# Kernel tuning notes

Measured on AMD Instinct MI355X. Metric: run time of the kernel, lower is better.

Reference implementation:

```python
import jax, jax.numpy as jnp
import numpy as np
import math

B, H, S, D = 8, 16, 1024, 64

def setup_inputs() -> dict:
    key = jax.random.key(0)
    kq, kk, kv = jax.random.split(key, 3)
    Q = jax.random.normal(kq, (B, H, S, D), dtype=jnp.float32)
    K = jax.random.normal(kk, (B, H, S, D), dtype=jnp.float32)
    V = jax.random.normal(kv, (B, H, S, D), dtype=jnp.float32)
    return {"Q": Q, "K": K, "V": V}

def reference(Q, K, V):
    d_k = K.shape[-1]
    # [B,H,S,S] attention scores
    score = jnp.einsum('bhqd,bhkd->bhqk', Q, K) / math.sqrt(d_k)
    attn = jax.nn.softmax(score, axis=-1)
    return jnp.einsum('bhqk,bhkd->bhqd', attn, V)
```

## Files before the change

### kernel.cpp

```cpp
#include <hip/hip_runtime.h>
#include <hip/hip_bf16.h>
#include <math.h>


#define S_ 1024
#define D_ 64
#define BQ 256
#define KVT 64
#define NTILE (S_ / KVT)
#define TILE_SHORTS (KVT * D_)

typedef __attribute__((ext_vector_type(8))) short bf16x8;
typedef __attribute__((ext_vector_type(4))) float f32x4;

#if __has_builtin(__builtin_amdgcn_exp2f)
#define EXP2F(x) __builtin_amdgcn_exp2f(x)
#else
#define EXP2F(x) exp2f(x)
#endif

__device__ __forceinline__ short f2bf(float f) {
    union { __hip_bfloat16 h; short s; } u;
    u.h = __float2bfloat16(f);
    return u.s;
}

__device__ __forceinline__ void gl2lds16(const short* g, short* l) {
    __builtin_amdgcn_global_load_lds(
        (const __attribute__((address_space(1))) unsigned int*)g,
        (__attribute__((address_space(3))) unsigned int*)l, 16, 0, 0);
}

__device__ __forceinline__ unsigned int pkbf(float a, float b) {
    unsigned int ua = __float_as_uint(a) + 0x8000u;
    unsigned int ub = __float_as_uint(b) + 0x8000u;
    return __builtin_amdgcn_perm(ub, ua, 0x07060302u);
}

__launch_bounds__(256)
__global__ void prepass_kernel(const float* __restrict__ K, const float* __restrict__ V,
                               short* __restrict__ Kb, short* __restrict__ Vb) {
    __shared__ __align__(16) short VtL[D_][72];
    const int tile = blockIdx.x, bh = blockIdx.y;
    const int tid = threadIdx.x;
    const int kv0 = tile * KVT;
    const size_t base = (size_t)bh * (S_ * D_);
    const float* Kp = K + base;
    const float* Vp = V + base;
    short* Kt = Kb + ((size_t)bh * NTILE + tile) * TILE_SHORTS;
    short* Vt = Vb + ((size_t)bh * NTILE + tile) * TILE_SHORTS;

    {
        const int c4 = tid & 15, g = tid >> 4;
        #pragma unroll
        for (int i = 0; i < 2; ++i) {
            const int kp = g + 16 * i;
            #pragma unroll
            for (int j = 0; j < 4; ++j) {
                const int d = c4 + 16 * j;
                float v0 = Vp[(size_t)(kv0 + 2 * kp) * D_ + d];
                float v1 = Vp[(size_t)(kv0 + 2 * kp + 1) * D_ + d];
                short2 vs; vs.x = f2bf(v0); vs.y = f2bf(v1);
                *(short2*)&VtL[d][2 * kp] = vs;
            }
        }
    }
    #pragma unroll
    for (int i = 0; i < 2; ++i) {
        const int s = tid + i * 256;
        const int mb = s >> 7, c = (s >> 6) & 1, lane = s & 63;
        const int quad = lane >> 4, l16 = lane & 15;
        const float* src = Kp + (size_t)(kv0 + mb * 16 + l16) * D_ + c * 32 + quad * 8;
        float4 a = *(const float4*)src;
        float4 b = *(const float4*)(src + 4);
        bf16x8 f;
        f[0]=f2bf(a.x); f[1]=f2bf(a.y); f[2]=f2bf(a.z); f[3]=f2bf(a.w);
        f[4]=f2bf(b.x); f[5]=f2bf(b.y); f[6]=f2bf(b.z); f[7]=f2bf(b.w);
        *(bf16x8*)&Kt[s * 8] = f;
    }
    __syncthreads();
    #pragma unroll
    for (int i = 0; i < 2; ++i) {
        const int s = tid + i * 256;
        const int t = s >> 7, c = (s >> 6) & 1, lane = s & 63;
        const int quad = lane >> 4, l16 = lane & 15;
        bf16x8 f = *(const bf16x8*)&VtL[t * 16 + l16][c * 32 + quad * 8];
        *(bf16x8*)&Vt[s * 8] = f;
    }
}

__launch_bounds__(256, 2)
__global__ void sdpa_kernel(const float* __restrict__ Q,
                            const short* __restrict__ Kb,
                            const short* __restrict__ Vb,
                            float* __restrict__ O) {
    __shared__ __align__(16) short Kbuf[2][TILE_SHORTS];
    __shared__ __align__(16) short Vbuf[2][TILE_SHORTS];
    __shared__ __align__(16) short Pfrag[4][1024];

    const int b   = blockIdx.x;
    const int bh  = (b & 7) | ((b >> 5) << 3);
    const int q0  = ((b >> 3) & 3) * BQ;
    const int tid = threadIdx.x;
    const int w = tid >> 6, lane = tid & 63;
    const int quad = lane >> 4, l16 = lane & 15;

    const size_t base = (size_t)bh * (S_ * D_);
    const float* Qp = Q + base;
    float*       Op = O + base;
    const short* Kg = Kb + (size_t)bh * NTILE * TILE_SHORTS;
    const short* Vg = Vb + (size_t)bh * NTILE * TILE_SHORTS;

    const float qs = 0.18033688011112042f;
    bf16x8 qfrag[4][2];
    #pragma unroll
    for (int nb = 0; nb < 4; ++nb) {
        const int qrow = q0 + w * 64 + nb * 16 + l16;
        #pragma unroll
        for (int c = 0; c < 2; ++c) {
            const float* src = Qp + (size_t)qrow * D_ + c * 32 + quad * 8;
            float4 a = *(const float4*)(src);
            float4 bb = *(const float4*)(src + 4);
            bf16x8 f;
            f[0]=f2bf(a.x*qs);  f[1]=f2bf(a.y*qs);  f[2]=f2bf(a.z*qs);  f[3]=f2bf(a.w*qs);
            f[4]=f2bf(bb.x*qs); f[5]=f2bf(bb.y*qs); f[6]=f2bf(bb.z*qs); f[7]=f2bf(bb.w*qs);
            qfrag[nb][c] = f;
        }
    }

    bf16x8 ones;
    #pragma unroll
    for (int i = 0; i < 8; ++i) ones[i] = (short)0x3F80;

    f32x4 l_acc[4];
    f32x4 o_acc[4][4];
    #pragma unroll
    for (int nb = 0; nb < 4; ++nb) {
        l_acc[nb] = (f32x4)0.f;
        #pragma unroll
        for (int t4 = 0; t4 < 4; ++t4)
            o_acc[nb][t4] = (f32x4)0.f;
    }

    auto stage = [&](int buf, int t) {
        const short* kt = Kg + (size_t)t * TILE_SHORTS;
        const short* vt = Vg + (size_t)t * TILE_SHORTS;
        #pragma unroll
        for (int i = 0; i < 2; ++i) {
            const int blk = i * 4 + w;
            gl2lds16(kt + (blk * 64 + lane) * 8, &Kbuf[buf][blk * 512]);
            gl2lds16(vt + (blk * 64 + lane) * 8, &Vbuf[buf][blk * 512]);
        }
    };

    stage(0, 0);
    __syncthreads();
    int cur = 0;

    #pragma unroll 1
    for (int t = 0; t < NTILE; ++t) {
        if (t + 1 < NTILE) stage(cur ^ 1, t + 1);

        bf16x8 kf[4][2], vf[4][2];
        #pragma unroll
        for (int mb = 0; mb < 4; ++mb) {
            kf[mb][0] = *(const bf16x8*)&Kbuf[cur][((mb * 2 + 0) * 64 + lane) * 8];
            kf[mb][1] = *(const bf16x8*)&Kbuf[cur][((mb * 2 + 1) * 64 + lane) * 8];
            vf[mb][0] = *(const bf16x8*)&Vbuf[cur][((mb * 2 + 0) * 64 + lane) * 8];
            vf[mb][1] = *(const bf16x8*)&Vbuf[cur][((mb * 2 + 1) * 64 + lane) * 8];
        }

        #pragma unroll
        for (int nb = 0; nb < 4; ++nb) {
            f32x4 st[4];
            #pragma unroll
            for (int mb = 0; mb < 4; ++mb) {
                f32x4 acc = (f32x4)0.f;
                acc = __builtin_amdgcn_mfma_f32_16x16x32_bf16(kf[mb][0], qfrag[nb][0], acc, 0, 0, 0);
                acc = __builtin_amdgcn_mfma_f32_16x16x32_bf16(kf[mb][1], qfrag[nb][1], acc, 0, 0, 0);
                st[mb] = acc;
            }

            #pragma unroll
            for (int mb = 0; mb < 4; ++mb) {
                float p0 = EXP2F(st[mb][0]);
                float p1 = EXP2F(st[mb][1]);
                float p2 = EXP2F(st[mb][2]);
                float p3 = EXP2F(st[mb][3]);
                uint2 pk;
                pk.x = pkbf(p0, p1);
                pk.y = pkbf(p2, p3);
                const int c  = mb >> 1;
                const int qp = (mb & 1) * 2 + (quad >> 1);
                const int j0 = (quad & 1) * 4;
                *(uint2*)&Pfrag[w][(c * 64 + qp * 16 + l16) * 8 + j0] = pk;
            }
            bf16x8 pf0 = *(const bf16x8*)&Pfrag[w][(0 * 64 + lane) * 8];
            bf16x8 pf1 = *(const bf16x8*)&Pfrag[w][(1 * 64 + lane) * 8];

            l_acc[nb] = __builtin_amdgcn_mfma_f32_16x16x32_bf16(pf0, ones, l_acc[nb], 0, 0, 0);
            l_acc[nb] = __builtin_amdgcn_mfma_f32_16x16x32_bf16(pf1, ones, l_acc[nb], 0, 0, 0);

            #pragma unroll
            for (int t4 = 0; t4 < 4; ++t4) {
                f32x4 acc = o_acc[nb][t4];
                acc = __builtin_amdgcn_mfma_f32_16x16x32_bf16(pf0, vf[t4][0], acc, 0, 0, 0);
                acc = __builtin_amdgcn_mfma_f32_16x16x32_bf16(pf1, vf[t4][1], acc, 0, 0, 0);
                o_acc[nb][t4] = acc;
            }
        }

        __syncthreads();
        cur ^= 1;
    }

    #pragma unroll
    for (int nb = 0; nb < 4; ++nb) {
        #pragma unroll
        for (int r = 0; r < 4; ++r) {
            const float inv = 1.0f / l_acc[nb][r];
            const int row = q0 + w * 64 + nb * 16 + quad * 4 + r;
            #pragma unroll
            for (int t4 = 0; t4 < 4; ++t4)
                Op[(size_t)row * D_ + t4 * 16 + l16] = o_acc[nb][t4][r] * inv;
        }
    }
}

extern "C" void kernel_launch(void* const* d_in, const int* in_sizes, int n_in,
                              void* d_out, int out_size, void* d_ws, size_t ws_size,
                              hipStream_t stream) {
    const float* Q = (const float*)d_in[0];
    const float* K = (const float*)d_in[1];
    const float* V = (const float*)d_in[2];
    float* O = (float*)d_out;

    const size_t tensor_shorts = (size_t)128 * NTILE * TILE_SHORTS;
    short* Kb = (short*)d_ws;
    short* Vb = Kb + tensor_shorts;

    dim3 pgrid(NTILE, 8 * 16);
    prepass_kernel<<<pgrid, dim3(256), 0, stream>>>(K, V, Kb, Vb);

    sdpa_kernel<<<dim3(512), dim3(256), 0, stream>>>(Q, Kb, Vb, O);
}
```

Measured before the change: 169.4 us.

## Load K/V fragments directly from global into registers, drop LDS staging and barriers

Removes the shared-memory double buffer for K and V along with the per-tile __syncthreads. Each wave now reads its K and V MFMA fragments straight from the pre-swizzled global buffers into registers, prefetching the next K tile one step ahead via ping-pong register arrays in a loop unrolled by two. The P scratch area is enlarged to one slot per nb, which may relax write-after-read ordering between iterations. Every wave now issues its own global loads, so K/V traffic through L2 rises fourfold, and register pressure grows with the extra prefetch arrays.

```diff
diff --git a/kernel.cpp b/kernel.cpp
--- a/kernel.cpp
+++ b/kernel.cpp
@@ -23,12 +23,6 @@
     union { __hip_bfloat16 h; short s; } u;
     u.h = __float2bfloat16(f);
     return u.s;
-}
-
-__device__ __forceinline__ void gl2lds16(const short* g, short* l) {
-    __builtin_amdgcn_global_load_lds(
-        (const __attribute__((address_space(1))) unsigned int*)g,
-        (__attribute__((address_space(3))) unsigned int*)l, 16, 0, 0);
 }
 
 __device__ __forceinline__ unsigned int pkbf(float a, float b) {
@@ -94,9 +88,7 @@
                             const short* __restrict__ Kb,
                             const short* __restrict__ Vb,
                             float* __restrict__ O) {
-    __shared__ __align__(16) short Kbuf[2][TILE_SHORTS];
-    __shared__ __align__(16) short Vbuf[2][TILE_SHORTS];
-    __shared__ __align__(16) short Pfrag[4][1024];
+    __shared__ __align__(16) short Pfrag[4][4][1024];
 
     const int b   = blockIdx.x;
     const int bh  = (b & 7) | ((b >> 5) << 3);
@@ -142,32 +134,23 @@
             o_acc[nb][t4] = (f32x4)0.f;
     }
 
-    auto stage = [&](int buf, int t) {
-        const short* kt = Kg + (size_t)t * TILE_SHORTS;
-        const short* vt = Vg + (size_t)t * TILE_SHORTS;
-        #pragma unroll
-        for (int i = 0; i < 2; ++i) {
-            const int blk = i * 4 + w;
-            gl2lds16(kt + (blk * 64 + lane) * 8, &Kbuf[buf][blk * 512]);
-            gl2lds16(vt + (blk * 64 + lane) * 8, &Vbuf[buf][blk * 512]);
-        }
-    };
-
-    stage(0, 0);
-    __syncthreads();
-    int cur = 0;
-
-    #pragma unroll 1
-    for (int t = 0; t < NTILE; ++t) {
-        if (t + 1 < NTILE) stage(cur ^ 1, t + 1);
-
-        bf16x8 kf[4][2], vf[4][2];
-        #pragma unroll
-        for (int mb = 0; mb < 4; ++mb) {
-            kf[mb][0] = *(const bf16x8*)&Kbuf[cur][((mb * 2 + 0) * 64 + lane) * 8];
-            kf[mb][1] = *(const bf16x8*)&Kbuf[cur][((mb * 2 + 1) * 64 + lane) * 8];
-            vf[mb][0] = *(const bf16x8*)&Vbuf[cur][((mb * 2 + 0) * 64 + lane) * 8];
-            vf[mb][1] = *(const bf16x8*)&Vbuf[cur][((mb * 2 + 1) * 64 + lane) * 8];
+    auto body = [&](bf16x8 (&kfc)[4][2], bf16x8 (&kfn)[4][2], int t) {
+        bf16x8 vf[4][2];
+        {
+            const short* vt = Vg + (size_t)t * TILE_SHORTS;
+            #pragma unroll
+            for (int mb = 0; mb < 4; ++mb) {
+                vf[mb][0] = *(const bf16x8*)(vt + ((mb * 2 + 0) * 64 + lane) * 8);
+                vf[mb][1] = *(const bf16x8*)(vt + ((mb * 2 + 1) * 64 + lane) * 8);
+            }
+        }
+        if (t + 1 < NTILE) {
+            const short* kt = Kg + (size_t)(t + 1) * TILE_SHORTS;
+            #pragma unroll
+            for (int mb = 0; mb < 4; ++mb) {
+                kfn[mb][0] = *(const bf16x8*)(kt + ((mb * 2 + 0) * 64 + lane) * 8);
+                kfn[mb][1] = *(const bf16x8*)(kt + ((mb * 2 + 1) * 64 + lane) * 8);
+            }
         }
 
         #pragma unroll
@@ -176,8 +159,8 @@
             #pragma unroll
             for (int mb = 0; mb < 4; ++mb) {
                 f32x4 acc = (f32x4)0.f;
-                acc = __builtin_amdgcn_mfma_f32_16x16x32_bf16(kf[mb][0], qfrag[nb][0], acc, 0, 0, 0);
-                acc = __builtin_amdgcn_mfma_f32_16x16x32_bf16(kf[mb][1], qfrag[nb][1], acc, 0, 0, 0);
+                acc = __builtin_amdgcn_mfma_f32_16x16x32_bf16(kfc[mb][0], qfrag[nb][0], acc, 0, 0, 0);
+                acc = __builtin_amdgcn_mfma_f32_16x16x32_bf16(kfc[mb][1], qfrag[nb][1], acc, 0, 0, 0);
                 st[mb] = acc;
             }
 
@@ -193,10 +176,10 @@
                 const int c  = mb >> 1;
                 const int qp = (mb & 1) * 2 + (quad >> 1);
                 const int j0 = (quad & 1) * 4;
-                *(uint2*)&Pfrag[w][(c * 64 + qp * 16 + l16) * 8 + j0] = pk;
-            }
-            bf16x8 pf0 = *(const bf16x8*)&Pfrag[w][(0 * 64 + lane) * 8];
-            bf16x8 pf1 = *(const bf16x8*)&Pfrag[w][(1 * 64 + lane) * 8];
+                *(uint2*)&Pfrag[w][nb][(c * 64 + qp * 16 + l16) * 8 + j0] = pk;
+            }
+            bf16x8 pf0 = *(const bf16x8*)&Pfrag[w][nb][(0 * 64 + lane) * 8];
+            bf16x8 pf1 = *(const bf16x8*)&Pfrag[w][nb][(1 * 64 + lane) * 8];
 
             l_acc[nb] = __builtin_amdgcn_mfma_f32_16x16x32_bf16(pf0, ones, l_acc[nb], 0, 0, 0);
             l_acc[nb] = __builtin_amdgcn_mfma_f32_16x16x32_bf16(pf1, ones, l_acc[nb], 0, 0, 0);
@@ -209,9 +192,19 @@
                 o_acc[nb][t4] = acc;
             }
         }
-
-        __syncthreads();
-        cur ^= 1;
+    };
+
+    bf16x8 kfA[4][2], kfB[4][2];
+    #pragma unroll
+    for (int mb = 0; mb < 4; ++mb) {
+        kfA[mb][0] = *(const bf16x8*)(Kg + ((mb * 2 + 0) * 64 + lane) * 8);
+        kfA[mb][1] = *(const bf16x8*)(Kg + ((mb * 2 + 1) * 64 + lane) * 8);
+    }
+
+    #pragma unroll 1
+    for (int tt = 0; tt < NTILE; tt += 2) {
+        body(kfA, kfB, tt);
+        body(kfB, kfA, tt + 1);
     }
 
     #pragma unroll
```

New measurement: 164.0 us. -3.2%, faster.
